# Kernel optimization log

Hardware: AMD Instinct MI355X
Metric: run time of the kernel (lower is better)

The kernel has to match this reference:

```python
import jax, jax.numpy as jnp
import numpy as np

B, R, D, G = 1024, 256, 512, 4
BETA_GROUP = 6.0
BETA_K = 8.0
INIT_KAPPA = 6.0


def setup_inputs() -> dict:
    key = jax.random.key(0)
    ks = jax.random.split(key, 9)
    f32 = jnp.float32
    return {
        "x": jax.random.normal(ks[0], (B, D), f32),
        "th": 0.1 * jax.random.normal(ks[1], (R, D), f32),
        "ineq_sign_param": 0.1 * jax.random.normal(ks[2], (R, D), f32),
        "e_sign_param": 0.1 * jax.random.normal(ks[3], (R, D), f32),
        "mask_logit": jnp.full((R, D), -2.0, f32) + 0.01 * jax.random.normal(ks[4], (R, D), f32),
        "log_kappa": jnp.asarray(np.log(INIT_KAPPA), f32),
        "group_logits": 0.1 * jax.random.normal(ks[5], (G, D), f32),
        "tg": 0.1 * jax.random.normal(ks[6], (R, G), f32),
        "gmask_logit": jnp.full((R, G), -1.0, f32) + 0.01 * jax.random.normal(ks[7], (R, G), f32),
        "k_frac_param": jnp.zeros((R,), f32),
        "head_w": 0.01 * jax.random.normal(ks[8], (1, R), f32),
        "head_b": jnp.zeros((1,), f32),
    }


def reference(x, th, ineq_sign_param, e_sign_param, mask_logit, log_kappa,
              group_logits, tg, gmask_logit, k_frac_param, head_w, head_b):
    kappa = jnp.clip(jnp.exp(log_kappa), 0.5, 50.0)
    ineq = jnp.tanh(ineq_sign_param)                       # (R, D)
    # c: (B, R, D) sharp per-feature comparison
    c = jax.nn.sigmoid(kappa * ineq[None] * (x[:, None, :] - th[None]))
    m = jax.nn.sigmoid(mask_logit)                         # (R, D)
    e_sign = jnp.tanh(e_sign_param)                        # (R, D)
    sym = (m * e_sign)[None] * (2.0 * c - 1.0)             # (B, R, D)
    A = jax.nn.softmax(group_logits, axis=0)               # (G, D)
    eg = jnp.einsum('brd,gd->brg', sym, A)                 # (B, R, G)
    pg = jax.nn.sigmoid(BETA_GROUP * (eg - tg[None]))
    gmask = jax.nn.sigmoid(gmask_logit)                    # (R, G)
    score = jnp.sum(pg * gmask[None], axis=2)              # (B, R)
    enabled = jnp.sum(gmask, axis=1)[None] + 1e-6          # (1, R)
    k = jax.nn.sigmoid(k_frac_param)[None] * enabled       # (1, R)
    z = jax.nn.sigmoid(BETA_K * (score - k))               # (B, R)
    y = z @ head_w.T + head_b                              # (B, 1)
    return y.squeeze(-1)
```

## Files before the change

### kernel.cpp

```cpp
#include <hip/hip_runtime.h>

#define B 1024
#define R 256
#define D 512
#define G 4

#define LOG2E 1.44269504088896340736f

#define OFF_PB   0
#define OFF_EPI  (R*64*48)
#define OFF_PART (OFF_EPI + R*12)
#define NRG 32
#define NBG 16

typedef float f2 __attribute__((ext_vector_type(2)));

static __device__ __forceinline__ f2 mk2(float a, float b) { f2 v; v.x = a; v.y = b; return v; }

__device__ __forceinline__ float sig_precise(float v) {
    return 1.0f / (1.0f + expf(-v));
}

__global__ __launch_bounds__(256)
void sge_precompute(const float* __restrict__ th,  const float* __restrict__ isp,
                    const float* __restrict__ esp, const float* __restrict__ ml,
                    const float* __restrict__ lk,  const float* __restrict__ gl,
                    const float* __restrict__ tg,  const float* __restrict__ gml,
                    const float* __restrict__ kf,  const float* __restrict__ hw,
                    float* __restrict__ ws)
{
    const int r   = blockIdx.x;
    const int tid = threadIdx.x;
    __shared__ float4 red[256];

    float kappa = expf(lk[0]);
    kappa = fminf(fmaxf(kappa, 0.5f), 50.0f);

    float4 psum = make_float4(0.f, 0.f, 0.f, 0.f);
    for (int d = tid; d < D; d += 256) {
        const int idx = r * D + d;
        const float thv  = th[idx];
        const float ineq = tanhf(isp[idx]);
        const float es   = tanhf(esp[idx]);
        const float mm   = sig_precise(ml[idx]);
        const float g0 = gl[0*D + d], g1 = gl[1*D + d], g2 = gl[2*D + d], g3 = gl[3*D + d];
        const float mx = fmaxf(fmaxf(g0, g1), fmaxf(g2, g3));
        const float e0 = expf(g0 - mx), e1 = expf(g1 - mx), e2 = expf(g2 - mx), e3 = expf(g3 - mx);
        const float inv = 1.0f / (e0 + e1 + e2 + e3);
        const float a0 = e0 * inv, a1 = e1 * inv, a2 = e2 * inv, a3 = e3 * inv;

        const float fa = -kappa * ineq * LOG2E;
        const float s  = mm * es;
        const float s0 = s * a0, s1 = s * a1, s2 = s * a2, s3 = s * a3;

        const int chunk = d >> 3, j = d & 7;
        float* pc = ws + OFF_PB + (size_t)(r * 64 + chunk) * 48;
        pc[j]      = thv;
        pc[8 + j]  = fa;
        pc[16 + j] = s0;
        pc[24 + j] = s1;
        pc[32 + j] = s2;
        pc[40 + j] = s3;
        psum.x += s0; psum.y += s1; psum.z += s2; psum.w += s3;
    }
    red[tid] = psum;
    __syncthreads();
    for (int s = 128; s > 0; s >>= 1) {
        if (tid < s) {
            red[tid].x += red[tid + s].x;
            red[tid].y += red[tid + s].y;
            red[tid].z += red[tid + s].z;
            red[tid].w += red[tid + s].w;
        }
        __syncthreads();
    }
    if (tid == 0) {
        const float4 base = red[0];
        const float gm0 = sig_precise(gml[r * G + 0]);
        const float gm1 = sig_precise(gml[r * G + 1]);
        const float gm2 = sig_precise(gml[r * G + 2]);
        const float gm3 = sig_precise(gml[r * G + 3]);
        const float en  = gm0 + gm1 + gm2 + gm3 + 1e-6f;
        const float k   = sig_precise(kf[r]) * en;
        float* epi = ws + OFF_EPI + r * 12;
        epi[0] = 6.0f * (base.x + tg[r * G + 0]) * LOG2E;
        epi[1] = 6.0f * (base.y + tg[r * G + 1]) * LOG2E;
        epi[2] = 6.0f * (base.z + tg[r * G + 2]) * LOG2E;
        epi[3] = 6.0f * (base.w + tg[r * G + 3]) * LOG2E;
        epi[4] = gm0; epi[5] = gm1; epi[6] = gm2; epi[7] = gm3;
        epi[8] = 8.0f * k * LOG2E;
        epi[9] = hw[r];
        epi[10] = 0.f; epi[11] = 0.f;
    }
}

__global__ __launch_bounds__(512, 4)
void sge_main(const float* __restrict__ x, const float* __restrict__ ws,
              float* __restrict__ part)
{
    __shared__ float xl[64 * 260];
    __shared__ float zbuf[512];

    const int tid  = threadIdx.x;
    const int lane = tid & 63;
    const int w    = __builtin_amdgcn_readfirstlane(tid >> 6);
    const int bg   = blockIdx.x;
    const int rg   = blockIdx.y;
    const int r    = rg * 8 + w;

    const float* pb = ws + OFF_PB + (size_t)r * (64 * 48);

    f2 acc0 = mk2(0.f, 0.f), acc1 = mk2(0.f, 0.f), acc2 = mk2(0.f, 0.f), acc3 = mk2(0.f, 0.f);

    float pA[48], pB[48];
    float4 xaA, xbA, xaB, xbB;

    auto compute = [&](const float (&p)[48], const float4& xa, const float4& xb) {
        const float xs[8] = {xa.x, xa.y, xa.z, xa.w, xb.x, xb.y, xb.z, xb.w};
        #pragma unroll
        for (int i = 0; i < 4; ++i) {
            const f2 xp  = mk2(xs[2*i],        xs[2*i + 1]);
            const f2 th2 = mk2(p[2*i],         p[2*i + 1]);
            const f2 fa2 = mk2(p[8  + 2*i],    p[9  + 2*i]);
            const f2 t   = (xp - th2) * fa2;
            f2 q;
            q.x = __builtin_amdgcn_exp2f(t.x);
            q.y = __builtin_amdgcn_exp2f(t.y);
            const f2 a = q + 1.0f;
            const float rp = __builtin_amdgcn_rcpf(a.x * a.y);
            const f2 c = mk2(a.y * rp, a.x * rp);
            acc0 = __builtin_elementwise_fma(mk2(p[16 + 2*i], p[17 + 2*i]), c, acc0);
            acc1 = __builtin_elementwise_fma(mk2(p[24 + 2*i], p[25 + 2*i]), c, acc1);
            acc2 = __builtin_elementwise_fma(mk2(p[32 + 2*i], p[33 + 2*i]), c, acc2);
            acc3 = __builtin_elementwise_fma(mk2(p[40 + 2*i], p[41 + 2*i]), c, acc3);
        }
    };

    for (int h = 0; h < 2; ++h) {
        __syncthreads();
        for (int i = tid; i < 64 * 64; i += 512) {
            const int row = i >> 6, c4 = i & 63;
            const float4 v = reinterpret_cast<const float4*>(x)[(bg * 64 + row) * (D / 4) + h * 64 + c4];
            *reinterpret_cast<float4*>(&xl[row * 260 + c4 * 4]) = v;
        }
        __syncthreads();

        {
            const float* pc = pb + (h * 32) * 48;
            #pragma unroll
            for (int j = 0; j < 48; ++j) pA[j] = pc[j];
            xaA = *reinterpret_cast<const float4*>(&xl[lane * 260 + 0]);
            xbA = *reinterpret_cast<const float4*>(&xl[lane * 260 + 4]);
        }
        #pragma unroll 1
        for (int c = 0; c < 32; c += 2) {
            {
                const float* pc = pb + (h * 32 + c + 1) * 48;
                #pragma unroll
                for (int j = 0; j < 48; ++j) pB[j] = pc[j];
                xaB = *reinterpret_cast<const float4*>(&xl[lane * 260 + (c + 1) * 8]);
                xbB = *reinterpret_cast<const float4*>(&xl[lane * 260 + (c + 1) * 8 + 4]);
            }
            compute(pA, xaA, xbA);
            {
                const int cn = (c + 2 < 32) ? (c + 2) : 0;
                const float* pc = pb + (h * 32 + cn) * 48;
                #pragma unroll
                for (int j = 0; j < 48; ++j) pA[j] = pc[j];
                xaA = *reinterpret_cast<const float4*>(&xl[lane * 260 + cn * 8]);
                xbA = *reinterpret_cast<const float4*>(&xl[lane * 260 + cn * 8 + 4]);
            }
            compute(pB, xaB, xbB);
        }
    }

    const float a0 = acc0.x + acc0.y;
    const float a1 = acc1.x + acc1.y;
    const float a2 = acc2.x + acc2.y;
    const float a3 = acc3.x + acc3.y;

    const float* epi = ws + OFF_EPI + r * 12;
    const float C12 = -12.0f * LOG2E;
    const float C8  = -8.0f  * LOG2E;
    const float pg0 = __builtin_amdgcn_rcpf(1.0f + __builtin_amdgcn_exp2f(fmaf(C12, a0, epi[0])));
    const float pg1 = __builtin_amdgcn_rcpf(1.0f + __builtin_amdgcn_exp2f(fmaf(C12, a1, epi[1])));
    const float pg2 = __builtin_amdgcn_rcpf(1.0f + __builtin_amdgcn_exp2f(fmaf(C12, a2, epi[2])));
    const float pg3 = __builtin_amdgcn_rcpf(1.0f + __builtin_amdgcn_exp2f(fmaf(C12, a3, epi[3])));
    float score = pg0 * epi[4];
    score = fmaf(pg1, epi[5], score);
    score = fmaf(pg2, epi[6], score);
    score = fmaf(pg3, epi[7], score);
    const float z = __builtin_amdgcn_rcpf(1.0f + __builtin_amdgcn_exp2f(fmaf(C8, score, epi[8])));
    zbuf[tid] = epi[9] * z;
    __syncthreads();
    if (tid < 64) {
        float s = zbuf[tid];
        #pragma unroll
        for (int ww = 1; ww < 8; ++ww) s += zbuf[ww * 64 + tid];
        part[rg * B + bg * 64 + tid] = s;
    }
}

__global__ __launch_bounds__(256)
void sge_finalize(const float* __restrict__ part, const float* __restrict__ hb,
                  float* __restrict__ y)
{
    const int b = blockIdx.x * 256 + threadIdx.x;
    float s = hb[0];
    #pragma unroll
    for (int rg = 0; rg < NRG; ++rg) s += part[rg * B + b];
    y[b] = s;
}

extern "C" void kernel_launch(void* const* d_in, const int* in_sizes, int n_in,
                              void* d_out, int out_size, void* d_ws, size_t ws_size,
                              hipStream_t stream)
{
    const float* x   = (const float*)d_in[0];
    const float* th  = (const float*)d_in[1];
    const float* isp = (const float*)d_in[2];
    const float* esp = (const float*)d_in[3];
    const float* ml  = (const float*)d_in[4];
    const float* lk  = (const float*)d_in[5];
    const float* gl  = (const float*)d_in[6];
    const float* tg  = (const float*)d_in[7];
    const float* gml = (const float*)d_in[8];
    const float* kf  = (const float*)d_in[9];
    const float* hw  = (const float*)d_in[10];
    const float* hb  = (const float*)d_in[11];
    float* ws = (float*)d_ws;
    float* y  = (float*)d_out;

    sge_precompute<<<R, 256, 0, stream>>>(th, isp, esp, ml, lk, gl, tg, gml, kf, hw, ws);
    sge_main<<<dim3(NBG, NRG), 512, 0, stream>>>(x, ws, ws + OFF_PART);
    sge_finalize<<<B / 256, 256, 0, stream>>>(ws + OFF_PART, hb, y);
}
```

Before: 55.83 us.

## Transpose x and split D across waves with broadcast params, batch-pair per lane

Adds a transpose kernel that writes x as D-major into workspace. The main kernel then reads x columns directly from global memory instead of staging tiles in LDS. Each lane now handles two batch rows while four waves split the D dimension for the same r, with per-r parameters repacked into 4-wide chunks that act as wave-uniform broadcasts, and partials are reduced in LDS. The grid grows to 8x128 blocks and finalize sums 128 partials. The aim is to cut the per-lane parameter register and load traffic, at the cost of an extra kernel launch and more partial-sum traffic.

```diff
diff --git a/kernel.cpp b/kernel.cpp
--- a/kernel.cpp
+++ b/kernel.cpp
@@ -8,17 +8,31 @@
 #define LOG2E 1.44269504088896340736f
 
 #define OFF_PB   0
-#define OFF_EPI  (R*64*48)
-#define OFF_PART (OFF_EPI + R*12)
-#define NRG 32
-#define NBG 16
+#define OFF_EPI  (R*128*24)
+#define OFF_XT   (OFF_EPI + R*16)
+#define OFF_PART (OFF_XT + D*B)
 
 typedef float f2 __attribute__((ext_vector_type(2)));
-
 static __device__ __forceinline__ f2 mk2(float a, float b) { f2 v; v.x = a; v.y = b; return v; }
+static __device__ __forceinline__ f2 mk2s(float a) { return mk2(a, a); }
 
 __device__ __forceinline__ float sig_precise(float v) {
     return 1.0f / (1.0f + expf(-v));
+}
+
+__global__ __launch_bounds__(256)
+void sge_transpose(const float* __restrict__ x, float* __restrict__ xT)
+{
+    __shared__ float t[64][65];
+    const int tid = threadIdx.x, tx = tid & 63, ty = tid >> 6;
+    const int d0 = blockIdx.x * 64, b0 = blockIdx.y * 64;
+    #pragma unroll
+    for (int i = 0; i < 64; i += 4)
+        t[ty + i][tx] = x[(size_t)(b0 + ty + i) * D + d0 + tx];
+    __syncthreads();
+    #pragma unroll
+    for (int i = 0; i < 64; i += 4)
+        xT[(size_t)(d0 + ty + i) * B + b0 + tx] = t[tx][ty + i];
 }
 
 __global__ __launch_bounds__(256)
@@ -53,14 +67,14 @@
         const float s  = mm * es;
         const float s0 = s * a0, s1 = s * a1, s2 = s * a2, s3 = s * a3;
 
-        const int chunk = d >> 3, j = d & 7;
-        float* pc = ws + OFF_PB + (size_t)(r * 64 + chunk) * 48;
+        const int chunk = d >> 2, j = d & 3;
+        float* pc = ws + OFF_PB + ((size_t)r * 128 + chunk) * 24;
         pc[j]      = thv;
-        pc[8 + j]  = fa;
-        pc[16 + j] = s0;
-        pc[24 + j] = s1;
-        pc[32 + j] = s2;
-        pc[40 + j] = s3;
+        pc[4 + j]  = fa;
+        pc[8 + j]  = s0;
+        pc[12 + j] = s1;
+        pc[16 + j] = s2;
+        pc[20 + j] = s3;
         psum.x += s0; psum.y += s1; psum.z += s2; psum.w += s3;
     }
     red[tid] = psum;
@@ -82,7 +96,7 @@
         const float gm3 = sig_precise(gml[r * G + 3]);
         const float en  = gm0 + gm1 + gm2 + gm3 + 1e-6f;
         const float k   = sig_precise(kf[r]) * en;
-        float* epi = ws + OFF_EPI + r * 12;
+        float* epi = ws + OFF_EPI + r * 16;
         epi[0] = 6.0f * (base.x + tg[r * G + 0]) * LOG2E;
         epi[1] = 6.0f * (base.y + tg[r * G + 1]) * LOG2E;
         epi[2] = 6.0f * (base.z + tg[r * G + 2]) * LOG2E;
@@ -90,114 +104,122 @@
         epi[4] = gm0; epi[5] = gm1; epi[6] = gm2; epi[7] = gm3;
         epi[8] = 8.0f * k * LOG2E;
         epi[9] = hw[r];
-        epi[10] = 0.f; epi[11] = 0.f;
+        epi[10] = 0.f; epi[11] = 0.f; epi[12] = 0.f;
+        epi[13] = 0.f; epi[14] = 0.f; epi[15] = 0.f;
     }
 }
 
 __global__ __launch_bounds__(512, 4)
-void sge_main(const float* __restrict__ x, const float* __restrict__ ws,
-              float* __restrict__ part)
-{
-    __shared__ float xl[64 * 260];
-    __shared__ float zbuf[512];
+void sge_main(const float* __restrict__ ws, float* __restrict__ part)
+{
+    __shared__ float lds1[6][64][8];
+    __shared__ float lds2[64][2];
 
     const int tid  = threadIdx.x;
     const int lane = tid & 63;
     const int w    = __builtin_amdgcn_readfirstlane(tid >> 6);
-    const int bg   = blockIdx.x;
+    const int dq   = w & 3;
+    const int rl   = w >> 2;
+    const int bt   = blockIdx.x;
     const int rg   = blockIdx.y;
-    const int r    = rg * 8 + w;
-
-    const float* pb = ws + OFF_PB + (size_t)r * (64 * 48);
-
-    f2 acc0 = mk2(0.f, 0.f), acc1 = mk2(0.f, 0.f), acc2 = mk2(0.f, 0.f), acc3 = mk2(0.f, 0.f);
-
-    float pA[48], pB[48];
-    float4 xaA, xbA, xaB, xbB;
-
-    auto compute = [&](const float (&p)[48], const float4& xa, const float4& xb) {
-        const float xs[8] = {xa.x, xa.y, xa.z, xa.w, xb.x, xb.y, xb.z, xb.w};
-        #pragma unroll
-        for (int i = 0; i < 4; ++i) {
-            const f2 xp  = mk2(xs[2*i],        xs[2*i + 1]);
-            const f2 th2 = mk2(p[2*i],         p[2*i + 1]);
-            const f2 fa2 = mk2(p[8  + 2*i],    p[9  + 2*i]);
-            const f2 t   = (xp - th2) * fa2;
+    const int r    = rg * 2 + rl;
+
+    const int b0 = bt * 128 + 2 * lane;
+    const float* xcol = ws + OFF_XT + (size_t)(dq * 128) * B + b0;
+
+    int pbyte = (int)(((size_t)r * 128 + (size_t)dq * 32) * 24 * 4);
+    asm volatile("" : "+v"(pbyte));
+    const char* pbase = (const char*)ws + pbyte;
+
+    f2 acc0 = mk2s(0.f), acc1 = mk2s(0.f), acc2 = mk2s(0.f), acc3 = mk2s(0.f);
+
+    float pA[24], pB[24];
+    f2 xA[4], xB[4];
+
+    auto loadP = [&](float (&p)[24], int c) {
+        const float4* q = reinterpret_cast<const float4*>(pbase + (size_t)c * 96);
+        #pragma unroll
+        for (int k = 0; k < 6; ++k) {
+            const float4 v = q[k];
+            p[4*k+0] = v.x; p[4*k+1] = v.y; p[4*k+2] = v.z; p[4*k+3] = v.w;
+        }
+    };
+    auto loadX = [&](f2 (&xv)[4], int c) {
+        #pragma unroll
+        for (int j = 0; j < 4; ++j)
+            xv[j] = *reinterpret_cast<const f2*>(xcol + (size_t)(c * 4 + j) * B);
+    };
+    auto compute = [&](const float (&p)[24], const f2 (&xv)[4]) {
+        #pragma unroll
+        for (int j = 0; j < 4; ++j) {
+            const f2 t = (xv[j] - mk2s(p[j])) * mk2s(p[4 + j]);
             f2 q;
             q.x = __builtin_amdgcn_exp2f(t.x);
             q.y = __builtin_amdgcn_exp2f(t.y);
             const f2 a = q + 1.0f;
             const float rp = __builtin_amdgcn_rcpf(a.x * a.y);
-            const f2 c = mk2(a.y * rp, a.x * rp);
-            acc0 = __builtin_elementwise_fma(mk2(p[16 + 2*i], p[17 + 2*i]), c, acc0);
-            acc1 = __builtin_elementwise_fma(mk2(p[24 + 2*i], p[25 + 2*i]), c, acc1);
-            acc2 = __builtin_elementwise_fma(mk2(p[32 + 2*i], p[33 + 2*i]), c, acc2);
-            acc3 = __builtin_elementwise_fma(mk2(p[40 + 2*i], p[41 + 2*i]), c, acc3);
+            const f2 c2 = mk2(a.y * rp, a.x * rp);
+            acc0 = __builtin_elementwise_fma(mk2s(p[8  + j]), c2, acc0);
+            acc1 = __builtin_elementwise_fma(mk2s(p[12 + j]), c2, acc1);
+            acc2 = __builtin_elementwise_fma(mk2s(p[16 + j]), c2, acc2);
+            acc3 = __builtin_elementwise_fma(mk2s(p[20 + j]), c2, acc3);
         }
     };
 
-    for (int h = 0; h < 2; ++h) {
-        __syncthreads();
-        for (int i = tid; i < 64 * 64; i += 512) {
-            const int row = i >> 6, c4 = i & 63;
-            const float4 v = reinterpret_cast<const float4*>(x)[(bg * 64 + row) * (D / 4) + h * 64 + c4];
-            *reinterpret_cast<float4*>(&xl[row * 260 + c4 * 4]) = v;
-        }
-        __syncthreads();
-
-        {
-            const float* pc = pb + (h * 32) * 48;
-            #pragma unroll
-            for (int j = 0; j < 48; ++j) pA[j] = pc[j];
-            xaA = *reinterpret_cast<const float4*>(&xl[lane * 260 + 0]);
-            xbA = *reinterpret_cast<const float4*>(&xl[lane * 260 + 4]);
-        }
-        #pragma unroll 1
-        for (int c = 0; c < 32; c += 2) {
-            {
-                const float* pc = pb + (h * 32 + c + 1) * 48;
-                #pragma unroll
-                for (int j = 0; j < 48; ++j) pB[j] = pc[j];
-                xaB = *reinterpret_cast<const float4*>(&xl[lane * 260 + (c + 1) * 8]);
-                xbB = *reinterpret_cast<const float4*>(&xl[lane * 260 + (c + 1) * 8 + 4]);
-            }
-            compute(pA, xaA, xbA);
-            {
-                const int cn = (c + 2 < 32) ? (c + 2) : 0;
-                const float* pc = pb + (h * 32 + cn) * 48;
-                #pragma unroll
-                for (int j = 0; j < 48; ++j) pA[j] = pc[j];
-                xaA = *reinterpret_cast<const float4*>(&xl[lane * 260 + cn * 8]);
-                xbA = *reinterpret_cast<const float4*>(&xl[lane * 260 + cn * 8 + 4]);
-            }
-            compute(pB, xaB, xbB);
-        }
-    }
-
-    const float a0 = acc0.x + acc0.y;
-    const float a1 = acc1.x + acc1.y;
-    const float a2 = acc2.x + acc2.y;
-    const float a3 = acc3.x + acc3.y;
-
-    const float* epi = ws + OFF_EPI + r * 12;
-    const float C12 = -12.0f * LOG2E;
-    const float C8  = -8.0f  * LOG2E;
-    const float pg0 = __builtin_amdgcn_rcpf(1.0f + __builtin_amdgcn_exp2f(fmaf(C12, a0, epi[0])));
-    const float pg1 = __builtin_amdgcn_rcpf(1.0f + __builtin_amdgcn_exp2f(fmaf(C12, a1, epi[1])));
-    const float pg2 = __builtin_amdgcn_rcpf(1.0f + __builtin_amdgcn_exp2f(fmaf(C12, a2, epi[2])));
-    const float pg3 = __builtin_amdgcn_rcpf(1.0f + __builtin_amdgcn_exp2f(fmaf(C12, a3, epi[3])));
-    float score = pg0 * epi[4];
-    score = fmaf(pg1, epi[5], score);
-    score = fmaf(pg2, epi[6], score);
-    score = fmaf(pg3, epi[7], score);
-    const float z = __builtin_amdgcn_rcpf(1.0f + __builtin_amdgcn_exp2f(fmaf(C8, score, epi[8])));
-    zbuf[tid] = epi[9] * z;
-    __syncthreads();
-    if (tid < 64) {
-        float s = zbuf[tid];
-        #pragma unroll
-        for (int ww = 1; ww < 8; ++ww) s += zbuf[ww * 64 + tid];
-        part[rg * B + bg * 64 + tid] = s;
+    loadP(pA, 0); loadX(xA, 0);
+    #pragma unroll 1
+    for (int c = 0; c < 32; c += 2) {
+        loadP(pB, c + 1); loadX(xB, c + 1);
+        compute(pA, xA);
+        const int cn = (c + 2 < 32) ? (c + 2) : 0;
+        loadP(pA, cn); loadX(xA, cn);
+        compute(pB, xB);
+    }
+
+    if (dq > 0) {
+        float* s = &lds1[rl * 3 + dq - 1][lane][0];
+        s[0] = acc0.x; s[1] = acc0.y; s[2] = acc1.x; s[3] = acc1.y;
+        s[4] = acc2.x; s[5] = acc2.y; s[6] = acc3.x; s[7] = acc3.y;
+    }
+    __syncthreads();
+
+    f2 contrib = mk2s(0.f);
+    if (dq == 0) {
+        #pragma unroll
+        for (int k = 0; k < 3; ++k) {
+            const float* s = &lds1[rl * 3 + k][lane][0];
+            acc0 += mk2(s[0], s[1]);
+            acc1 += mk2(s[2], s[3]);
+            acc2 += mk2(s[4], s[5]);
+            acc3 += mk2(s[6], s[7]);
+        }
+        const float* epi = ws + OFF_EPI + r * 16;
+        const float C12 = -12.0f * LOG2E;
+        const float C8  = -8.0f  * LOG2E;
+        auto sigmoid2 = [&](f2 t) {
+            f2 q;
+            q.x = __builtin_amdgcn_exp2f(t.x);
+            q.y = __builtin_amdgcn_exp2f(t.y);
+            const f2 a = q + 1.0f;
+            const float rp = __builtin_amdgcn_rcpf(a.x * a.y);
+            return mk2(a.y * rp, a.x * rp);
+        };
+        const f2 pg0 = sigmoid2(__builtin_elementwise_fma(acc0, mk2s(C12), mk2s(epi[0])));
+        const f2 pg1 = sigmoid2(__builtin_elementwise_fma(acc1, mk2s(C12), mk2s(epi[1])));
+        const f2 pg2 = sigmoid2(__builtin_elementwise_fma(acc2, mk2s(C12), mk2s(epi[2])));
+        const f2 pg3 = sigmoid2(__builtin_elementwise_fma(acc3, mk2s(C12), mk2s(epi[3])));
+        f2 score = pg0 * mk2s(epi[4]);
+        score = __builtin_elementwise_fma(pg1, mk2s(epi[5]), score);
+        score = __builtin_elementwise_fma(pg2, mk2s(epi[6]), score);
+        score = __builtin_elementwise_fma(pg3, mk2s(epi[7]), score);
+        const f2 z = sigmoid2(__builtin_elementwise_fma(score, mk2s(C8), mk2s(epi[8])));
+        contrib = mk2s(epi[9]) * z;
+    }
+    if (w == 4) { lds2[lane][0] = contrib.x; lds2[lane][1] = contrib.y; }
+    __syncthreads();
+    if (w == 0) {
+        const f2 tot = contrib + mk2(lds2[lane][0], lds2[lane][1]);
+        *reinterpret_cast<f2*>(part + (size_t)rg * B + b0) = tot;
     }
 }
 
@@ -207,8 +229,8 @@
 {
     const int b = blockIdx.x * 256 + threadIdx.x;
     float s = hb[0];
-    #pragma unroll
-    for (int rg = 0; rg < NRG; ++rg) s += part[rg * B + b];
+    #pragma unroll 8
+    for (int k = 0; k < 128; ++k) s += part[(size_t)k * B + b];
     y[b] = s;
 }
 
@@ -231,7 +253,8 @@
     float* ws = (float*)d_ws;
     float* y  = (float*)d_out;
 
+    sge_transpose<<<dim3(D / 64, B / 64), 256, 0, stream>>>(x, ws + OFF_XT);
     sge_precompute<<<R, 256, 0, stream>>>(th, isp, esp, ml, lk, gl, tg, gml, kf, hw, ws);
-    sge_main<<<dim3(NBG, NRG), 512, 0, stream>>>(x, ws, ws + OFF_PART);
+    sge_main<<<dim3(8, 128), 512, 0, stream>>>(ws, ws + OFF_PART);
     sge_finalize<<<B / 256, 256, 0, stream>>>(ws + OFF_PART, hb, y);
 }
```

Measured after the change: 104.1 us. 1.86x slower.

## Split D across two blocks per row group and move nonlinear epilogue to finalize

Applied to the files above, without the earlier changes.

The main kernel grid doubles by splitting the feature dimension into two halves. Each block handles 256 features instead of 512, with half the shared memory and a higher occupancy hint. Per-rule group accumulators are written to workspace, and the finalize kernel sums the two halves and applies the sigmoid/score/head epilogue. This is meant to fill more compute units, since there were only 512 blocks before. In exchange it adds global traffic for the partial accumulators and moves a serial per-rule loop into a finalize kernel with only 16 blocks.

```diff
diff --git a/kernel.cpp b/kernel.cpp
--- a/kernel.cpp
+++ b/kernel.cpp
@@ -10,11 +10,9 @@
 #define OFF_PB   0
 #define OFF_EPI  (R*64*48)
 #define OFF_PART (OFF_EPI + R*12)
-#define NRG 32
 #define NBG 16
 
 typedef float f2 __attribute__((ext_vector_type(2)));
-
 static __device__ __forceinline__ f2 mk2(float a, float b) { f2 v; v.x = a; v.y = b; return v; }
 
 __device__ __forceinline__ float sig_precise(float v) {
@@ -94,18 +92,20 @@
     }
 }
 
-__global__ __launch_bounds__(512, 4)
+__global__ __launch_bounds__(512, 8)
 void sge_main(const float* __restrict__ x, const float* __restrict__ ws,
               float* __restrict__ part)
 {
-    __shared__ float xl[64 * 260];
+    __shared__ float xl[64 * 132];
     __shared__ float zbuf[512];
 
     const int tid  = threadIdx.x;
     const int lane = tid & 63;
     const int w    = __builtin_amdgcn_readfirstlane(tid >> 6);
     const int bg   = blockIdx.x;
-    const int rg   = blockIdx.y;
+    const int rgdh = blockIdx.y;
+    const int rg   = rgdh >> 1;
+    const int dh   = rgdh & 1;
     const int r    = rg * 8 + w;
 
     const float* pb = ws + OFF_PB + (size_t)r * (64 * 48);
@@ -119,9 +119,9 @@
         const float xs[8] = {xa.x, xa.y, xa.z, xa.w, xb.x, xb.y, xb.z, xb.w};
         #pragma unroll
         for (int i = 0; i < 4; ++i) {
-            const f2 xp  = mk2(xs[2*i],        xs[2*i + 1]);
-            const f2 th2 = mk2(p[2*i],         p[2*i + 1]);
-            const f2 fa2 = mk2(p[8  + 2*i],    p[9  + 2*i]);
+            const f2 xp  = mk2(xs[2*i],     xs[2*i + 1]);
+            const f2 th2 = mk2(p[2*i],      p[2*i + 1]);
+            const f2 fa2 = mk2(p[8 + 2*i],  p[9 + 2*i]);
             const f2 t   = (xp - th2) * fa2;
             f2 q;
             q.x = __builtin_amdgcn_exp2f(t.x);
@@ -136,39 +136,42 @@
         }
     };
 
-    for (int h = 0; h < 2; ++h) {
+    for (int qtr = 0; qtr < 2; ++qtr) {
+        const int doff = dh * 256 + qtr * 128;
         __syncthreads();
-        for (int i = tid; i < 64 * 64; i += 512) {
-            const int row = i >> 6, c4 = i & 63;
-            const float4 v = reinterpret_cast<const float4*>(x)[(bg * 64 + row) * (D / 4) + h * 64 + c4];
-            *reinterpret_cast<float4*>(&xl[row * 260 + c4 * 4]) = v;
+        for (int i = tid; i < 64 * 32; i += 512) {
+            const int row = i >> 5, c4 = i & 31;
+            const float4 v = *reinterpret_cast<const float4*>(
+                &x[(size_t)(bg * 64 + row) * D + doff + c4 * 4]);
+            *reinterpret_cast<float4*>(&xl[row * 132 + c4 * 4]) = v;
         }
         __syncthreads();
 
+        const int cb = dh * 32 + qtr * 16;
         {
-            const float* pc = pb + (h * 32) * 48;
+            const float* pc = pb + (size_t)cb * 48;
             #pragma unroll
             for (int j = 0; j < 48; ++j) pA[j] = pc[j];
-            xaA = *reinterpret_cast<const float4*>(&xl[lane * 260 + 0]);
-            xbA = *reinterpret_cast<const float4*>(&xl[lane * 260 + 4]);
+            xaA = *reinterpret_cast<const float4*>(&xl[lane * 132 + 0]);
+            xbA = *reinterpret_cast<const float4*>(&xl[lane * 132 + 4]);
         }
         #pragma unroll 1
-        for (int c = 0; c < 32; c += 2) {
+        for (int c = 0; c < 16; c += 2) {
             {
-                const float* pc = pb + (h * 32 + c + 1) * 48;
+                const float* pc = pb + (size_t)(cb + c + 1) * 48;
                 #pragma unroll
                 for (int j = 0; j < 48; ++j) pB[j] = pc[j];
-                xaB = *reinterpret_cast<const float4*>(&xl[lane * 260 + (c + 1) * 8]);
-                xbB = *reinterpret_cast<const float4*>(&xl[lane * 260 + (c + 1) * 8 + 4]);
+                xaB = *reinterpret_cast<const float4*>(&xl[lane * 132 + (c + 1) * 8]);
+                xbB = *reinterpret_cast<const float4*>(&xl[lane * 132 + (c + 1) * 8 + 4]);
             }
             compute(pA, xaA, xbA);
             {
-                const int cn = (c + 2 < 32) ? (c + 2) : 0;
-                const float* pc = pb + (h * 32 + cn) * 48;
+                const int cn = (c + 2 < 16) ? (c + 2) : 0;
+                const float* pc = pb + (size_t)(cb + cn) * 48;
                 #pragma unroll
                 for (int j = 0; j < 48; ++j) pA[j] = pc[j];
-                xaA = *reinterpret_cast<const float4*>(&xl[lane * 260 + cn * 8]);
-                xbA = *reinterpret_cast<const float4*>(&xl[lane * 260 + cn * 8 + 4]);
+                xaA = *reinterpret_cast<const float4*>(&xl[lane * 132 + cn * 8]);
+                xbA = *reinterpret_cast<const float4*>(&xl[lane * 132 + cn * 8 + 4]);
             }
             compute(pB, xaB, xbB);
         }
@@ -179,37 +182,53 @@
     const float a2 = acc2.x + acc2.y;
     const float a3 = acc3.x + acc3.y;
 
-    const float* epi = ws + OFF_EPI + r * 12;
+    {
+        float* pa = part + ((((size_t)rg * 2 + dh) * 8 + w) * 16 + bg) * 64 * 4 + lane * 4;
+        pa[0] = a0; pa[1] = a1; pa[2] = a2; pa[3] = a3;
+    }
+    (void)zbuf;
+}
+
+__global__ __launch_bounds__(256)
+void sge_finalize(const float* __restrict__ part, const float* __restrict__ ws,
+                  const float* __restrict__ hb, float* __restrict__ y)
+{
+    __shared__ float red[256];
+    const int tid  = threadIdx.x;
+    const int lane = tid & 63;
+    const int slice = tid >> 6;
+    const int bg   = blockIdx.x;
     const float C12 = -12.0f * LOG2E;
     const float C8  = -8.0f  * LOG2E;
-    const float pg0 = __builtin_amdgcn_rcpf(1.0f + __builtin_amdgcn_exp2f(fmaf(C12, a0, epi[0])));
-    const float pg1 = __builtin_amdgcn_rcpf(1.0f + __builtin_amdgcn_exp2f(fmaf(C12, a1, epi[1])));
-    const float pg2 = __builtin_amdgcn_rcpf(1.0f + __builtin_amdgcn_exp2f(fmaf(C12, a2, epi[2])));
-    const float pg3 = __builtin_amdgcn_rcpf(1.0f + __builtin_amdgcn_exp2f(fmaf(C12, a3, epi[3])));
-    float score = pg0 * epi[4];
-    score = fmaf(pg1, epi[5], score);
-    score = fmaf(pg2, epi[6], score);
-    score = fmaf(pg3, epi[7], score);
-    const float z = __builtin_amdgcn_rcpf(1.0f + __builtin_amdgcn_exp2f(fmaf(C8, score, epi[8])));
-    zbuf[tid] = epi[9] * z;
+
+    float s = 0.f;
+    for (int rr = 0; rr < 64; ++rr) {
+        const int r  = slice * 64 + rr;
+        const int rg = r >> 3, w = r & 7;
+        const float* p0 = part + ((((size_t)rg * 2 + 0) * 8 + w) * 16 + bg) * 64 * 4 + lane * 4;
+        const float* p1 = part + ((((size_t)rg * 2 + 1) * 8 + w) * 16 + bg) * 64 * 4 + lane * 4;
+        const float a0 = p0[0] + p1[0];
+        const float a1 = p0[1] + p1[1];
+        const float a2 = p0[2] + p1[2];
+        const float a3 = p0[3] + p1[3];
+        const float* epi = ws + OFF_EPI + r * 12;
+        const float pg0 = __builtin_amdgcn_rcpf(1.0f + __builtin_amdgcn_exp2f(fmaf(C12, a0, epi[0])));
+        const float pg1 = __builtin_amdgcn_rcpf(1.0f + __builtin_amdgcn_exp2f(fmaf(C12, a1, epi[1])));
+        const float pg2 = __builtin_amdgcn_rcpf(1.0f + __builtin_amdgcn_exp2f(fmaf(C12, a2, epi[2])));
+        const float pg3 = __builtin_amdgcn_rcpf(1.0f + __builtin_amdgcn_exp2f(fmaf(C12, a3, epi[3])));
+        float score = pg0 * epi[4];
+        score = fmaf(pg1, epi[5], score);
+        score = fmaf(pg2, epi[6], score);
+        score = fmaf(pg3, epi[7], score);
+        const float z = __builtin_amdgcn_rcpf(1.0f + __builtin_amdgcn_exp2f(fmaf(C8, score, epi[8])));
+        s = fmaf(epi[9], z, s);
+    }
+    red[tid] = s;
     __syncthreads();
-    if (tid < 64) {
-        float s = zbuf[tid];
-        #pragma unroll
-        for (int ww = 1; ww < 8; ++ww) s += zbuf[ww * 64 + tid];
-        part[rg * B + bg * 64 + tid] = s;
-    }
-}
-
-__global__ __launch_bounds__(256)
-void sge_finalize(const float* __restrict__ part, const float* __restrict__ hb,
-                  float* __restrict__ y)
-{
-    const int b = blockIdx.x * 256 + threadIdx.x;
-    float s = hb[0];
-    #pragma unroll
-    for (int rg = 0; rg < NRG; ++rg) s += part[rg * B + b];
-    y[b] = s;
+    if (slice == 0) {
+        const float tot = hb[0] + red[lane] + red[64 + lane] + red[128 + lane] + red[192 + lane];
+        y[bg * 64 + lane] = tot;
+    }
 }
 
 extern "C" void kernel_launch(void* const* d_in, const int* in_sizes, int n_in,
@@ -232,6 +251,6 @@
     float* y  = (float*)d_out;
 
     sge_precompute<<<R, 256, 0, stream>>>(th, isp, esp, ml, lk, gl, tg, gml, kf, hw, ws);
-    sge_main<<<dim3(NBG, NRG), 512, 0, stream>>>(x, ws, ws + OFF_PART);
-    sge_finalize<<<B / 256, 256, 0, stream>>>(ws + OFF_PART, hb, y);
-}
+    sge_main<<<dim3(NBG, 64), 512, 0, stream>>>(x, ws, ws + OFF_PART);
+    sge_finalize<<<NBG, 256, 0, stream>>>(ws + OFF_PART, ws, hb, y);
+}
```

Measured after the change: 70.37 us. +26.0%, slower.
